# Kernel optimization log

Hardware: AMD Instinct MI355X
Metric: run time of the kernel (lower is better)

The kernel has to match this reference:

```python
import jax, jax.numpy as jnp
import numpy as np

RADIUS = 0.05  # screen-space splat radius (NDC units), from raster_settings


def setup_inputs() -> dict:
    key = jax.random.key(0)
    k1, k2, k3 = jax.random.split(key, 3)
    B, N, C, H = 1, 4096, 8, 128
    # camera-space points: z in [2,4], xy chosen so NDC projection (x/z) covers [-1,1]
    z = jax.random.uniform(k1, (B, N, 1), minval=2.0, maxval=4.0)
    xy = jax.random.uniform(k2, (B, N, 2), minval=-1.0, maxval=1.0) * z
    points = jnp.concatenate([xy, z], axis=-1)  # [B,N,3]
    features = jax.random.normal(k3, (B, N, C), dtype=jnp.float32)
    return {"points": points, "features": features, "image_size": H, "points_per_pixel": 8}


def reference(points, features, image_size, points_per_pixel):
    B, N, _ = points.shape
    H = W = image_size
    K = points_per_pixel
    C = features.shape[-1]
    r2 = RADIUS * RADIUS

    x, y, z = points[..., 0], points[..., 1], points[..., 2]
    # perspective projection to NDC (focal length 1)
    px = x / z  # [B,N]
    py = y / z

    # pixel centers in NDC [-1,1]
    xs = (jnp.arange(W, dtype=jnp.float32) + 0.5) / W * 2.0 - 1.0
    ys = (jnp.arange(H, dtype=jnp.float32) + 0.5) / H * 2.0 - 1.0
    gy, gx = jnp.meshgrid(ys, xs, indexing="ij")
    gx = gx.reshape(-1)  # [P], P = H*W
    gy = gy.reshape(-1)

    # squared screen-space distance pixel<->point: [B, P, N]
    dx = gx[None, :, None] - px[:, None, :]
    dy = gy[None, :, None] - py[:, None, :]
    dist2 = dx * dx + dy * dy

    hit = (dist2 < r2) & (z[:, None, :] > 0.0)
    NEG = jnp.float32(-1e30)
    # K nearest-in-depth points per pixel among hits (top_k of -z)
    keys = jnp.where(hit, -z[:, None, :], NEG)
    negz, idx = jax.lax.top_k(keys, K)  # [B,P,K]
    valid = negz > NEG * 0.5

    d2k = jnp.take_along_axis(dist2, idx, axis=2)           # [B,P,K]
    fk = jax.vmap(lambda f, i: f[i])(features, idx)          # [B,P,K,C]

    # AlphaCompositor: w = 1 - d2/r^2, front-to-back compositing
    alpha = jnp.where(valid, jnp.clip(1.0 - d2k / r2, 0.0, 1.0), 0.0)
    trans = jnp.cumprod(1.0 - alpha, axis=-1)
    T = jnp.concatenate([jnp.ones_like(alpha[..., :1]), trans[..., :-1]], axis=-1)
    w = alpha * T                                            # [B,P,K]

    out = jnp.einsum("bpk,bpkc->bpc", w, fk)
    return out.reshape(B, H, W, C)
```

## Files before the change

### kernel.cpp

```cpp
#include <hip/hip_runtime.h>
#include <math.h>

#define RADIUS 0.05f
#define NSLICE 8
#define SPCAP 1024
#define HCAP  40
#define HSTR  41

__global__ __launch_bounds__(512) void render_tiles(
    const float* __restrict__ points,
    const float* __restrict__ features,
    float* __restrict__ out,
    int N, int H, int W, int tiles_x)
{
    const float r2 = RADIUS * RADIUS;
    const float inv_r2 = 1.0f / r2;

    __shared__ float4 sp[SPCAP];
    __shared__ float  s_hz[64 * HSTR];
    __shared__ float  s_hd[64 * HSTR];
    __shared__ int    s_hi[64 * HSTR];
    __shared__ int    s_pcnt[64];
    __shared__ int    s_cnt;

    if (threadIdx.x == 0) s_cnt = 0;
    if (threadIdx.x < 64) s_pcnt[threadIdx.x] = 0;
    __syncthreads();

    const int tile = blockIdx.x;
    const int tx = tile % tiles_x;
    const int ty = tile / tiles_x;
    const int x0i = tx * 8;
    const int y0i = ty * 8;

    const float sx = 2.0f / (float)W;
    const float sy = 2.0f / (float)H;
    const float bx0 = ((float)x0i + 0.5f) * sx - 1.0f - RADIUS;
    const float bx1 = ((float)(x0i + 7) + 0.5f) * sx - 1.0f + RADIUS;
    const float by0 = ((float)y0i + 0.5f) * sy - 1.0f - RADIUS;
    const float by1 = ((float)(y0i + 7) + 0.5f) * sy - 1.0f + RADIUS;

    for (int i = threadIdx.x; i < N; i += 512) {
        float x = points[3 * i + 0];
        float y = points[3 * i + 1];
        float z = points[3 * i + 2];
        float px = x / z;
        float py = y / z;
        bool keep = (z > 0.0f) & (px >= bx0) & (px <= bx1) & (py >= by0) & (py <= by1);
        if (keep) {
            int pos = atomicAdd(&s_cnt, 1);
            if (pos < SPCAP) sp[pos] = make_float4(px, py, z, __int_as_float(i));
        }
    }
    __syncthreads();
    const int cnt = min(s_cnt, SPCAP);

    const int pxl = threadIdx.x & 63;
    const int slice = threadIdx.x >> 6;
    const int lx = pxl & 7;
    const int ly = pxl >> 3;
    const int ix = x0i + lx;
    const int iy = y0i + ly;
    const float gx = ((float)ix + 0.5f) * sx - 1.0f;
    const float gy = ((float)iy + 0.5f) * sy - 1.0f;

    for (int c = slice; c < cnt; c += NSLICE) {
        float4 q = sp[c];
        float dx = gx - q.x;
        float dy = gy - q.y;
        float d2 = dx * dx + dy * dy;
        if (d2 < r2) {
            int pos = atomicAdd(&s_pcnt[pxl], 1);
            if (pos < HCAP) {
                s_hz[pxl * HSTR + pos] = q.z;
                s_hd[pxl * HSTR + pos] = d2;
                s_hi[pxl * HSTR + pos] = __float_as_int(q.w);
            }
        }
    }
    __syncthreads();

    if (threadIdx.x < 64) {
        const int m = min(s_pcnt[pxl], HCAP);
        float zk[8];
        int sk[8];
#pragma unroll
        for (int k = 0; k < 8; k++) { zk[k] = 3.0e38f; sk[k] = 0; }

        for (int i = 0; i < m; i++) {
            float z = s_hz[pxl * HSTR + i];
            if (z < zk[7]) {
                int s = i;
#pragma unroll
                for (int k = 0; k < 8; k++) {
                    bool lt = z < zk[k];
                    float tz = zk[k];
                    int ts = sk[k];
                    if (lt) { zk[k] = z; sk[k] = s; z = tz; s = ts; }
                }
            }
        }

        float acc0 = 0.f, acc1 = 0.f, acc2 = 0.f, acc3 = 0.f;
        float acc4 = 0.f, acc5 = 0.f, acc6 = 0.f, acc7 = 0.f;
        float T = 1.0f;
#pragma unroll
        for (int k = 0; k < 8; k++) {
            if (zk[k] < 1.0e30f) {
                float d2 = s_hd[pxl * HSTR + sk[k]];
                int   id = s_hi[pxl * HSTR + sk[k]];
                float alpha = 1.0f - d2 * inv_r2;
                alpha = fminf(fmaxf(alpha, 0.0f), 1.0f);
                float w = alpha * T;
                T *= (1.0f - alpha);
                const float4* f = (const float4*)(features + (size_t)id * 8);
                float4 f0 = f[0];
                float4 f1 = f[1];
                acc0 += w * f0.x; acc1 += w * f0.y; acc2 += w * f0.z; acc3 += w * f0.w;
                acc4 += w * f1.x; acc5 += w * f1.y; acc6 += w * f1.z; acc7 += w * f1.w;
            }
        }

        if (ix < W && iy < H) {
            float4* o = (float4*)(out + (size_t)(iy * W + ix) * 8);
            o[0] = make_float4(acc0, acc1, acc2, acc3);
            o[1] = make_float4(acc4, acc5, acc6, acc7);
        }
    }
}

extern "C" void kernel_launch(void* const* d_in, const int* in_sizes, int n_in,
                              void* d_out, int out_size, void* d_ws, size_t ws_size,
                              hipStream_t stream) {
    const float* points = (const float*)d_in[0];
    const float* features = (const float*)d_in[1];
    float* out = (float*)d_out;

    int N = in_sizes[0] / 3;
    int C = in_sizes[1] / N;
    int P = out_size / C;
    int H = (int)(sqrt((double)P) + 0.5);
    int W = H;
    int tiles_x = (W + 7) / 8;
    int tiles_y = (H + 7) / 8;

    render_tiles<<<tiles_x * tiles_y, 512, 0, stream>>>(points, features, out, N, H, W, tiles_x);
}
```

Before: 72.45 us.

## Double block size, cull without divides, and prefetch shared-memory loads

Raises the block size from 512 to 1024 threads and the pixel slices from 8 to 16, so each tile's point cull and hit test spread over more threads. The culling test now multiplies the bounds by z instead of dividing, and a fast reciprocal is computed only for points that survive. The hit-test and top-K loops prefetch the next shared-memory element (software pipelining). The per-tile point capacity drops from 1024 to 256, which risks silently dropping candidates in dense tiles, and the larger block may lower occupancy.

```diff
diff --git a/kernel.cpp b/kernel.cpp
--- a/kernel.cpp
+++ b/kernel.cpp
@@ -2,12 +2,13 @@
 #include <math.h>
 
 #define RADIUS 0.05f
-#define NSLICE 8
-#define SPCAP 1024
-#define HCAP  40
-#define HSTR  41
+#define NTHREADS 1024
+#define NSLICE   16
+#define SPCAP   256
+#define HCAP    40
+#define HSTR    41
 
-__global__ __launch_bounds__(512) void render_tiles(
+__global__ __launch_bounds__(1024) void render_tiles(
     const float* __restrict__ points,
     const float* __restrict__ features,
     float* __restrict__ out,
@@ -30,26 +31,23 @@
     const int tile = blockIdx.x;
     const int tx = tile % tiles_x;
     const int ty = tile / tiles_x;
-    const int x0i = tx * 8;
-    const int y0i = ty * 8;
-
-    const float sx = 2.0f / (float)W;
-    const float sy = 2.0f / (float)H;
+    const int x0i = tx * 8, y0i = ty * 8;
+    const float sx = 2.0f / (float)W, sy = 2.0f / (float)H;
     const float bx0 = ((float)x0i + 0.5f) * sx - 1.0f - RADIUS;
     const float bx1 = ((float)(x0i + 7) + 0.5f) * sx - 1.0f + RADIUS;
     const float by0 = ((float)y0i + 0.5f) * sy - 1.0f - RADIUS;
     const float by1 = ((float)(y0i + 7) + 0.5f) * sy - 1.0f + RADIUS;
 
-    for (int i = threadIdx.x; i < N; i += 512) {
+    for (int i = threadIdx.x; i < N; i += NTHREADS) {
         float x = points[3 * i + 0];
         float y = points[3 * i + 1];
         float z = points[3 * i + 2];
-        float px = x / z;
-        float py = y / z;
-        bool keep = (z > 0.0f) & (px >= bx0) & (px <= bx1) & (py >= by0) & (py <= by1);
+        bool keep = (z > 0.0f) & (x >= bx0 * z) & (x <= bx1 * z)
+                               & (y >= by0 * z) & (y <= by1 * z);
         if (keep) {
+            float rz = __builtin_amdgcn_rcpf(z);
             int pos = atomicAdd(&s_cnt, 1);
-            if (pos < SPCAP) sp[pos] = make_float4(px, py, z, __int_as_float(i));
+            if (pos < SPCAP) sp[pos] = make_float4(x * rz, y * rz, z, __int_as_float(i));
         }
     }
     __syncthreads();
@@ -57,25 +55,31 @@
 
     const int pxl = threadIdx.x & 63;
     const int slice = threadIdx.x >> 6;
-    const int lx = pxl & 7;
-    const int ly = pxl >> 3;
-    const int ix = x0i + lx;
-    const int iy = y0i + ly;
+    const int ix = x0i + (pxl & 7);
+    const int iy = y0i + (pxl >> 3);
     const float gx = ((float)ix + 0.5f) * sx - 1.0f;
     const float gy = ((float)iy + 0.5f) * sy - 1.0f;
 
-    for (int c = slice; c < cnt; c += NSLICE) {
+    int c = slice;
+    if (c < cnt) {
         float4 q = sp[c];
-        float dx = gx - q.x;
-        float dy = gy - q.y;
-        float d2 = dx * dx + dy * dy;
-        if (d2 < r2) {
-            int pos = atomicAdd(&s_pcnt[pxl], 1);
-            if (pos < HCAP) {
-                s_hz[pxl * HSTR + pos] = q.z;
-                s_hd[pxl * HSTR + pos] = d2;
-                s_hi[pxl * HSTR + pos] = __float_as_int(q.w);
+        while (true) {
+            int cn = c + NSLICE;
+            bool more = cn < cnt;
+            float4 qn = sp[more ? cn : slice];
+            float dx = gx - q.x;
+            float dy = gy - q.y;
+            float d2 = dx * dx + dy * dy;
+            if (d2 < r2) {
+                int pos = atomicAdd(&s_pcnt[pxl], 1);
+                if (pos < HCAP) {
+                    s_hz[pxl * HSTR + pos] = q.z;
+                    s_hd[pxl * HSTR + pos] = d2;
+                    s_hi[pxl * HSTR + pos] = __float_as_int(q.w);
+                }
             }
+            if (!more) break;
+            q = qn; c = cn;
         }
     }
     __syncthreads();
@@ -87,8 +91,10 @@
 #pragma unroll
         for (int k = 0; k < 8; k++) { zk[k] = 3.0e38f; sk[k] = 0; }
 
+        float z_next = s_hz[pxl * HSTR];
         for (int i = 0; i < m; i++) {
-            float z = s_hz[pxl * HSTR + i];
+            float z = z_next;
+            z_next = s_hz[pxl * HSTR + i + 1];
             if (z < zk[7]) {
                 int s = i;
 #pragma unroll
@@ -144,5 +150,6 @@
     int tiles_x = (W + 7) / 8;
     int tiles_y = (H + 7) / 8;
 
-    render_tiles<<<tiles_x * tiles_y, 512, 0, stream>>>(points, features, out, N, H, W, tiles_x);
+    render_tiles<<<tiles_x * tiles_y, NTHREADS, 0, stream>>>(points, features, out,
+                                                             N, H, W, tiles_x);
 }
```

Result: no change. 71.70 us (-1.0%).
